# Performance work log

Measured on AMD Instinct MI355X. Metric: run time of the kernel, lower is better.

The kernel has to match this reference:

```python
import jax, jax.numpy as jnp
import numpy as np

NUM_EXPERTS = 8
TOP_K = 2


def setup_inputs() -> dict:
    key = jax.random.key(0)
    ks = jax.random.split(key, 5)
    B, L, E, H, N = 2, 2048, 1024, 2048, NUM_EXPERTS
    return {
        "x": jax.random.normal(ks[0], (B, L, E), dtype=jnp.float32),
        "gate_kernel": jax.random.normal(ks[1], (E, N), dtype=jnp.float32) / np.sqrt(E),
        "w0_kernel": jax.random.normal(ks[2], (N, E, H), dtype=jnp.float32) / np.sqrt(E),
        "w1_kernel": jax.random.normal(ks[3], (N, E, H), dtype=jnp.float32) / np.sqrt(E),
        "wo_kernel": jax.random.normal(ks[4], (N, H, E), dtype=jnp.float32) / np.sqrt(H),
    }


def reference(x, gate_kernel, w0_kernel, w1_kernel, wo_kernel):
    B, L, E = x.shape
    # Router: [B, L, N]
    gate_logits = jnp.einsum("ble,en->bln", x, gate_kernel)
    top_k_weights, top_k_indices = jax.lax.top_k(gate_logits, TOP_K)
    # softmax over the selected top-k logits (in fp32, as in original)
    softmax_probs = jax.nn.softmax(top_k_weights.astype(jnp.float32), axis=-1)
    # scatter probs back into dense [B, L, N] routing weights
    weights = jnp.zeros_like(gate_logits)
    b_idx = jnp.arange(B)[:, None, None]
    l_idx = jnp.arange(L)[:, None]
    weights = weights.at[b_idx, l_idx, top_k_indices].set(softmax_probs)
    # Dense all-experts FFN (as in the original module)
    layer_w0 = jnp.einsum("ble,neh->blnh", x, w0_kernel)  # [B,L,N,H]
    layer_w1 = jnp.einsum("ble,neh->blnh", x, w1_kernel)
    layer_mult = jax.nn.silu(layer_w0) * layer_w1
    intermediate = jnp.einsum("blnh,nhe->blne", layer_mult, wo_kernel)
    output = jnp.einsum("blne,bln->ble", intermediate, weights)
    return output
```

## Files before the change

kernel.cpp:

```cpp
#include <hip/hip_runtime.h>
#include <stdint.h>


#define T_TOKENS 4096
#define E_DIM 1024
#define H_DIM 2048
#define BM 128
#define BN 64
#define BK 32
#define MAX_TILES 72

typedef __attribute__((ext_vector_type(8))) short bf16x8;
typedef __attribute__((ext_vector_type(8))) unsigned short u16x8;
typedef __attribute__((ext_vector_type(4))) float f32x4;

__device__ __forceinline__ unsigned short f2bf(float f) {
  unsigned u = __float_as_uint(f);
  u += 0x7fff + ((u >> 16) & 1);
  return (unsigned short)(u >> 16);
}

__device__ __forceinline__ void gll16(const void* g, void* l) {
  __builtin_amdgcn_global_load_lds(
      (__attribute__((address_space(1))) void*)(uintptr_t)g,
      (__attribute__((address_space(3))) void*)l, 16, 0, 0);
}

__global__ __launch_bounds__(256) void router_kernel(
    const float* __restrict__ x, const float* __restrict__ gate,
    int* __restrict__ cnt, int2* __restrict__ tok_e,
    int2* __restrict__ tok_pos, float2* __restrict__ tok_w,
    unsigned short* __restrict__ xb) {
  int lane = threadIdx.x & 63;
  int wv = threadIdx.x >> 6;
  int t = blockIdx.x * 4 + wv;
  const float* xr = x + (size_t)t * E_DIM;
  unsigned short* xbr = xb + (size_t)t * E_DIM;
  float acc[8];
#pragma unroll
  for (int n = 0; n < 8; n++) acc[n] = 0.f;
#pragma unroll
  for (int i = 0; i < 16; i++) {
    int k = i * 64 + lane;
    float xv = xr[k];
    xbr[k] = f2bf(xv);
    const float4* gp = (const float4*)(gate + (size_t)k * 8);
    float4 g0 = gp[0], g1 = gp[1];
    acc[0] += xv * g0.x; acc[1] += xv * g0.y;
    acc[2] += xv * g0.z; acc[3] += xv * g0.w;
    acc[4] += xv * g1.x; acc[5] += xv * g1.y;
    acc[6] += xv * g1.z; acc[7] += xv * g1.w;
  }
#pragma unroll
  for (int s = 32; s >= 1; s >>= 1) {
#pragma unroll
    for (int n = 0; n < 8; n++) acc[n] += __shfl_xor(acc[n], s, 64);
  }
  if (lane == 0) {
    int i0 = 0; float v0 = acc[0];
#pragma unroll
    for (int n = 1; n < 8; n++) if (acc[n] > v0) { v0 = acc[n]; i0 = n; }
    int i1 = -1; float v1 = -3.4e38f;
#pragma unroll
    for (int n = 0; n < 8; n++) if (n != i0 && acc[n] > v1) { v1 = acc[n]; i1 = n; }
    float e1 = __expf(v1 - v0);
    float inv = 1.f / (1.f + e1);
    int p0 = atomicAdd(&cnt[i0], 1);
    int p1 = atomicAdd(&cnt[i1], 1);
    tok_e[t] = make_int2(i0, i1);
    tok_pos[t] = make_int2(p0, p1);
    tok_w[t] = make_float2(inv, e1 * inv);
  }
}

__global__ __launch_bounds__(256) void scatter_kernel(
    const int* __restrict__ cnt, const int2* __restrict__ tok_e,
    const int2* __restrict__ tok_pos, int* __restrict__ tlist,
    int2* __restrict__ tok_slot) {
  int t = blockIdx.x * 256 + threadIdx.x;
  if (t >= T_TOKENS) return;
  int offs[8]; int a = 0;
#pragma unroll
  for (int e = 0; e < 8; e++) { offs[e] = a; a += cnt[e]; }
  int2 te = tok_e[t]; int2 tp = tok_pos[t];
  int s0 = offs[te.x] + tp.x, s1 = offs[te.y] + tp.y;
  tlist[s0] = t; tlist[s1] = t;
  tok_slot[t] = make_int2(s0, s1);
}

__global__ __launch_bounds__(256) void transpose_convert_kernel(
    const float* __restrict__ src, unsigned short* __restrict__ dst, int R, int C) {
  __shared__ float tile[64][65];
  size_t bofs = (size_t)blockIdx.z * R * C;
  const float* s = src + bofs;
  unsigned short* d = dst + bofs;
  int r0 = blockIdx.y * 64, c0 = blockIdx.x * 64;
  int tr = threadIdx.x >> 2;
  int tc = (threadIdx.x & 3) * 16;
  const float* sp = s + (size_t)(r0 + tr) * C + c0 + tc;
#pragma unroll
  for (int j = 0; j < 4; j++) {
    float4 v = ((const float4*)sp)[j];
    tile[tr][tc + j * 4 + 0] = v.x; tile[tr][tc + j * 4 + 1] = v.y;
    tile[tr][tc + j * 4 + 2] = v.z; tile[tr][tc + j * 4 + 3] = v.w;
  }
  __syncthreads();
  int co = tr;
  int rc = tc;
  u16x8 o0, o1;
#pragma unroll
  for (int j = 0; j < 8; j++) o0[j] = f2bf(tile[rc + j][co]);
#pragma unroll
  for (int j = 0; j < 8; j++) o1[j] = f2bf(tile[rc + 8 + j][co]);
  unsigned short* dp = d + (size_t)(c0 + co) * R + r0 + rc;
  *(u16x8*)dp = o0;
  *(u16x8*)(dp + 8) = o1;
}

__device__ __forceinline__ bool map_tile(const int* cnt, int tile, int& eSel,
                                         int& slot0, int& rows) {
  eSel = -1;
  int acc = 0, off = 0;
  for (int e = 0; e < 8; e++) {
    int ce = cnt[e];
    int te = (ce + BM - 1) / BM;
    if (eSel < 0 && tile < acc + te) {
      eSel = e;
      int tin = tile - acc;
      slot0 = off + tin * BM;
      rows = min(BM, ce - tin * BM);
    }
    acc += te; off += ce;
  }
  return eSel >= 0;
}

__global__ __launch_bounds__(256, 3) void gemm1_kernel(
    const unsigned short* __restrict__ xb,
    const unsigned short* __restrict__ w0t,
    const unsigned short* __restrict__ w1t,
    const int* __restrict__ cnt, const int* __restrict__ tlist,
    unsigned short* __restrict__ Mbuf) {
  __shared__ alignas(16) unsigned short As[BM * BK];
  __shared__ alignas(16) unsigned short B0s[BN * BK];
  __shared__ alignas(16) unsigned short B1s[BN * BK];

  int eSel, slot0, rows;
  if (!map_tile(cnt, blockIdx.y, eSel, slot0, rows)) return;
  int h0 = blockIdx.x * BN;

  int tid = threadIdx.x, lane = tid & 63, wv = tid >> 6;
  int sr = lane >> 2;
  int colE = (lane & 3) * 8;
  int ar0 = wv * 32 + sr, ar1 = ar0 + 16;
  int ra0 = min(ar0, rows - 1), ra1 = min(ar1, rows - 1);
  const unsigned short* aS0 = xb + (size_t)tlist[slot0 + ra0] * E_DIM + colE;
  const unsigned short* aS1 = xb + (size_t)tlist[slot0 + ra1] * E_DIM + colE;
  int br = wv * 16 + sr;
  const unsigned short* b0S = w0t + ((size_t)eSel * H_DIM + h0 + br) * E_DIM + colE;
  const unsigned short* b1S = w1t + ((size_t)eSel * H_DIM + h0 + br) * E_DIM + colE;

  f32x4 acc0[4][2], acc1[4][2];
  f32x4 fz = {0.f, 0.f, 0.f, 0.f};
#pragma unroll
  for (int m = 0; m < 4; m++)
#pragma unroll
    for (int n = 0; n < 2; n++) { acc0[m][n] = fz; acc1[m][n] = fz; }

  unsigned short* As_w = &As[wv * 1024];
  unsigned short* B0s_w = &B0s[wv * 512];
  unsigned short* B1s_w = &B1s[wv * 512];
  int rbase = (wv >> 1) * 64, cbase = (wv & 1) * 32;
  int fr = lane & 15, fk = (lane >> 4) * 8;

  for (int k0 = 0; k0 < E_DIM; k0 += BK) {
    gll16(aS0 + k0, As_w);
    gll16(aS1 + k0, As_w + 512);
    gll16(b0S + k0, B0s_w);
    gll16(b1S + k0, B1s_w);
    __syncthreads();
    bf16x8 a[4], b0[2], b1[2];
#pragma unroll
    for (int m = 0; m < 4; m++)
      a[m] = *(const bf16x8*)&As[(rbase + m * 16 + fr) * BK + fk];
#pragma unroll
    for (int n = 0; n < 2; n++) {
      b0[n] = *(const bf16x8*)&B0s[(cbase + n * 16 + fr) * BK + fk];
      b1[n] = *(const bf16x8*)&B1s[(cbase + n * 16 + fr) * BK + fk];
    }
#pragma unroll
    for (int m = 0; m < 4; m++)
#pragma unroll
      for (int n = 0; n < 2; n++) {
        acc0[m][n] = __builtin_amdgcn_mfma_f32_16x16x32_bf16(a[m], b0[n], acc0[m][n], 0, 0, 0);
        acc1[m][n] = __builtin_amdgcn_mfma_f32_16x16x32_bf16(a[m], b1[n], acc1[m][n], 0, 0, 0);
      }
    __syncthreads();
  }
  int rj = (lane >> 4) * 4;
#pragma unroll
  for (int m = 0; m < 4; m++) {
#pragma unroll
    for (int j = 0; j < 4; j++) {
      int r = rbase + m * 16 + rj + j;
      if (r < rows) {
        size_t rowp = (size_t)(slot0 + r) * H_DIM + h0 + cbase + fr;
#pragma unroll
        for (int n = 0; n < 2; n++) {
          float v0 = acc0[m][n][j], v1 = acc1[m][n][j];
          float mv = v0 / (1.f + __expf(-v0)) * v1;
          Mbuf[rowp + n * 16] = f2bf(mv);
        }
      }
    }
  }
}

__global__ __launch_bounds__(256, 4) void gemm2_kernel(
    const unsigned short* __restrict__ Mbuf,
    const unsigned short* __restrict__ wot,
    const int* __restrict__ cnt,
    float* __restrict__ Obuf) {
  __shared__ alignas(16) unsigned short As[BM * BK];
  __shared__ alignas(16) unsigned short Bs[BN * BK];

  int eSel, slot0, rows;
  if (!map_tile(cnt, blockIdx.y, eSel, slot0, rows)) return;
  int eo0 = blockIdx.x * BN;

  int tid = threadIdx.x, lane = tid & 63, wv = tid >> 6;
  int sr = lane >> 2;
  int colE = (lane & 3) * 8;
  int ar0 = wv * 32 + sr, ar1 = ar0 + 16;
  int ra0 = min(ar0, rows - 1), ra1 = min(ar1, rows - 1);
  const unsigned short* aS0 = Mbuf + (size_t)(slot0 + ra0) * H_DIM + colE;
  const unsigned short* aS1 = Mbuf + (size_t)(slot0 + ra1) * H_DIM + colE;
  int br = wv * 16 + sr;
  const unsigned short* bS = wot + ((size_t)eSel * E_DIM + eo0 + br) * H_DIM + colE;

  f32x4 acc[4][2];
  f32x4 fz = {0.f, 0.f, 0.f, 0.f};
#pragma unroll
  for (int m = 0; m < 4; m++)
#pragma unroll
    for (int n = 0; n < 2; n++) acc[m][n] = fz;

  unsigned short* As_w = &As[wv * 1024];
  unsigned short* Bs_w = &Bs[wv * 512];
  int rbase = (wv >> 1) * 64, cbase = (wv & 1) * 32;
  int fr = lane & 15, fk = (lane >> 4) * 8;

  for (int k0 = 0; k0 < H_DIM; k0 += BK) {
    gll16(aS0 + k0, As_w);
    gll16(aS1 + k0, As_w + 512);
    gll16(bS + k0, Bs_w);
    __syncthreads();
    bf16x8 a[4], b[2];
#pragma unroll
    for (int m = 0; m < 4; m++)
      a[m] = *(const bf16x8*)&As[(rbase + m * 16 + fr) * BK + fk];
#pragma unroll
    for (int n = 0; n < 2; n++)
      b[n] = *(const bf16x8*)&Bs[(cbase + n * 16 + fr) * BK + fk];
#pragma unroll
    for (int m = 0; m < 4; m++)
#pragma unroll
      for (int n = 0; n < 2; n++)
        acc[m][n] = __builtin_amdgcn_mfma_f32_16x16x32_bf16(a[m], b[n], acc[m][n], 0, 0, 0);
    __syncthreads();
  }
  int rj = (lane >> 4) * 4;
#pragma unroll
  for (int m = 0; m < 4; m++) {
#pragma unroll
    for (int j = 0; j < 4; j++) {
      int r = rbase + m * 16 + rj + j;
      if (r < rows) {
        size_t rowp = (size_t)(slot0 + r) * E_DIM + eo0 + cbase + fr;
#pragma unroll
        for (int n = 0; n < 2; n++) Obuf[rowp + n * 16] = acc[m][n][j];
      }
    }
  }
}

__global__ __launch_bounds__(256) void combine_kernel(
    const float* __restrict__ Obuf, const int2* __restrict__ tok_slot,
    const float2* __restrict__ tok_w, float* __restrict__ out) {
  int t = blockIdx.x;
  int c = threadIdx.x * 4;
  int2 s = tok_slot[t];
  float2 wgt = tok_w[t];
  float4 a = *(const float4*)(Obuf + (size_t)s.x * E_DIM + c);
  float4 b = *(const float4*)(Obuf + (size_t)s.y * E_DIM + c);
  float4 o;
  o.x = wgt.x * a.x + wgt.y * b.x;
  o.y = wgt.x * a.y + wgt.y * b.y;
  o.z = wgt.x * a.z + wgt.y * b.z;
  o.w = wgt.x * a.w + wgt.y * b.w;
  *(float4*)(out + (size_t)t * E_DIM + c) = o;
}

extern "C" void kernel_launch(void* const* d_in, const int* in_sizes, int n_in,
                              void* d_out, int out_size, void* d_ws, size_t ws_size,
                              hipStream_t stream) {
  (void)in_sizes; (void)n_in; (void)out_size; (void)ws_size;
  const float* x = (const float*)d_in[0];
  const float* gate = (const float*)d_in[1];
  const float* w0 = (const float*)d_in[2];
  const float* w1 = (const float*)d_in[3];
  const float* wo = (const float*)d_in[4];
  float* out = (float*)d_out;
  char* ws = (char*)d_ws;

  int* cnt = (int*)(ws + 0);
  int2* tok_e = (int2*)(ws + 256);
  int2* tok_pos = (int2*)(ws + 256 + 32768);
  float2* tok_w = (float2*)(ws + 256 + 2 * 32768);
  int2* tok_slot = (int2*)(ws + 256 + 3 * 32768);
  int* tlist = (int*)(ws + 256 + 4 * 32768);
  size_t o = 256 + 5 * 32768;
  unsigned short* xb = (unsigned short*)(ws + o);  o += (size_t)T_TOKENS * E_DIM * 2;
  unsigned short* w0t = (unsigned short*)(ws + o); o += (size_t)8 * H_DIM * E_DIM * 2;
  unsigned short* w1t = (unsigned short*)(ws + o); o += (size_t)8 * H_DIM * E_DIM * 2;
  unsigned short* wot = (unsigned short*)(ws + o); o += (size_t)8 * E_DIM * H_DIM * 2;
  unsigned short* Mbuf = (unsigned short*)(ws + o); o += (size_t)8192 * H_DIM * 2;
  float* Obuf = (float*)w0t;

  hipMemsetAsync(cnt, 0, 32, stream);
  hipLaunchKernelGGL(router_kernel, dim3(1024), dim3(256), 0, stream,
                     x, gate, cnt, tok_e, tok_pos, tok_w, xb);
  hipLaunchKernelGGL(scatter_kernel, dim3(16), dim3(256), 0, stream,
                     cnt, tok_e, tok_pos, tlist, tok_slot);
  hipLaunchKernelGGL(transpose_convert_kernel, dim3(32, 16, 8), dim3(256), 0, stream,
                     w0, w0t, E_DIM, H_DIM);
  hipLaunchKernelGGL(transpose_convert_kernel, dim3(32, 16, 8), dim3(256), 0, stream,
                     w1, w1t, E_DIM, H_DIM);
  hipLaunchKernelGGL(transpose_convert_kernel, dim3(16, 32, 8), dim3(256), 0, stream,
                     wo, wot, H_DIM, E_DIM);
  hipLaunchKernelGGL(gemm1_kernel, dim3(32, MAX_TILES), dim3(256), 0, stream,
                     xb, w0t, w1t, cnt, tlist, Mbuf);
  hipLaunchKernelGGL(gemm2_kernel, dim3(16, MAX_TILES), dim3(256), 0, stream,
                     Mbuf, wot, cnt, Obuf);
  hipLaunchKernelGGL(combine_kernel, dim3(4096), dim3(256), 0, stream,
                     Obuf, tok_slot, tok_w, out);
}
```

Baseline: 501.2 us.

## Fuse combine into gemm2 via atomics, widen BK with swizzled LDS, vectorize router

```diff
diff --git a/kernel.cpp b/kernel.cpp
--- a/kernel.cpp
+++ b/kernel.cpp
@@ -6,8 +6,7 @@
 #define E_DIM 1024
 #define H_DIM 2048
 #define BM 128
-#define BN 64
-#define BK 32
+#define BK 64
 #define MAX_TILES 72
 
 typedef __attribute__((ext_vector_type(8))) short bf16x8;
@@ -25,6 +24,7 @@
       (__attribute__((address_space(1))) void*)(uintptr_t)g,
       (__attribute__((address_space(3))) void*)l, 16, 0, 0);
 }
+
 
 __global__ __launch_bounds__(256) void router_kernel(
     const float* __restrict__ x, const float* __restrict__ gate,
@@ -40,16 +40,22 @@
 #pragma unroll
   for (int n = 0; n < 8; n++) acc[n] = 0.f;
 #pragma unroll
-  for (int i = 0; i < 16; i++) {
-    int k = i * 64 + lane;
-    float xv = xr[k];
-    xbr[k] = f2bf(xv);
-    const float4* gp = (const float4*)(gate + (size_t)k * 8);
-    float4 g0 = gp[0], g1 = gp[1];
-    acc[0] += xv * g0.x; acc[1] += xv * g0.y;
-    acc[2] += xv * g0.z; acc[3] += xv * g0.w;
-    acc[4] += xv * g1.x; acc[5] += xv * g1.y;
-    acc[6] += xv * g1.z; acc[7] += xv * g1.w;
+  for (int i = 0; i < 4; i++) {
+    int k4 = i * 256 + lane * 4;
+    float4 xv = *(const float4*)(xr + k4);
+    ushort4 ov;
+    ov.x = f2bf(xv.x); ov.y = f2bf(xv.y); ov.z = f2bf(xv.z); ov.w = f2bf(xv.w);
+    *(ushort4*)(xbr + k4) = ov;
+    float xa[4] = {xv.x, xv.y, xv.z, xv.w};
+#pragma unroll
+    for (int c = 0; c < 4; c++) {
+      const float4* gp = (const float4*)(gate + (size_t)(k4 + c) * 8);
+      float4 g0 = gp[0], g1 = gp[1];
+      acc[0] += xa[c] * g0.x; acc[1] += xa[c] * g0.y;
+      acc[2] += xa[c] * g0.z; acc[3] += xa[c] * g0.w;
+      acc[4] += xa[c] * g1.x; acc[5] += xa[c] * g1.y;
+      acc[6] += xa[c] * g1.z; acc[7] += xa[c] * g1.w;
+    }
   }
 #pragma unroll
   for (int s = 32; s >= 1; s >>= 1) {
@@ -75,17 +81,18 @@
 
 __global__ __launch_bounds__(256) void scatter_kernel(
     const int* __restrict__ cnt, const int2* __restrict__ tok_e,
-    const int2* __restrict__ tok_pos, int* __restrict__ tlist,
-    int2* __restrict__ tok_slot) {
+    const int2* __restrict__ tok_pos, const float2* __restrict__ tok_w,
+    int* __restrict__ tlist, float* __restrict__ wlist) {
   int t = blockIdx.x * 256 + threadIdx.x;
   if (t >= T_TOKENS) return;
   int offs[8]; int a = 0;
 #pragma unroll
   for (int e = 0; e < 8; e++) { offs[e] = a; a += cnt[e]; }
   int2 te = tok_e[t]; int2 tp = tok_pos[t];
+  float2 w = tok_w[t];
   int s0 = offs[te.x] + tp.x, s1 = offs[te.y] + tp.y;
   tlist[s0] = t; tlist[s1] = t;
-  tok_slot[t] = make_int2(s0, s1);
+  wlist[s0] = w.x; wlist[s1] = w.y;
 }
 
 __global__ __launch_bounds__(256) void transpose_convert_kernel(
@@ -142,23 +149,32 @@
     const int* __restrict__ cnt, const int* __restrict__ tlist,
     unsigned short* __restrict__ Mbuf) {
   __shared__ alignas(16) unsigned short As[BM * BK];
-  __shared__ alignas(16) unsigned short B0s[BN * BK];
-  __shared__ alignas(16) unsigned short B1s[BN * BK];
+  __shared__ alignas(16) unsigned short B0s[64 * BK];
+  __shared__ alignas(16) unsigned short B1s[64 * BK];
 
   int eSel, slot0, rows;
   if (!map_tile(cnt, blockIdx.y, eSel, slot0, rows)) return;
-  int h0 = blockIdx.x * BN;
+  int h0 = blockIdx.x * 64;
 
   int tid = threadIdx.x, lane = tid & 63, wv = tid >> 6;
-  int sr = lane >> 2;
-  int colE = (lane & 3) * 8;
-  int ar0 = wv * 32 + sr, ar1 = ar0 + 16;
-  int ra0 = min(ar0, rows - 1), ra1 = min(ar1, rows - 1);
-  const unsigned short* aS0 = xb + (size_t)tlist[slot0 + ra0] * E_DIM + colE;
-  const unsigned short* aS1 = xb + (size_t)tlist[slot0 + ra1] * E_DIM + colE;
-  int br = wv * 16 + sr;
-  const unsigned short* b0S = w0t + ((size_t)eSel * H_DIM + h0 + br) * E_DIM + colE;
-  const unsigned short* b1S = w1t + ((size_t)eSel * H_DIM + h0 + br) * E_DIM + colE;
+  int lr = lane >> 3;
+  int swz = ((lane & 7) ^ lr) * 8;
+
+  const unsigned short* aP[4];
+#pragma unroll
+  for (int j = 0; j < 4; j++) {
+    int r = wv * 32 + j * 8 + lr;
+    int rc = min(r, rows - 1);
+    aP[j] = xb + (size_t)tlist[slot0 + rc] * E_DIM + swz;
+  }
+  const unsigned short* b0P[2];
+  const unsigned short* b1P[2];
+#pragma unroll
+  for (int j = 0; j < 2; j++) {
+    int hr = h0 + wv * 16 + j * 8 + lr;
+    b0P[j] = w0t + ((size_t)eSel * H_DIM + hr) * E_DIM + swz;
+    b1P[j] = w1t + ((size_t)eSel * H_DIM + hr) * E_DIM + swz;
+  }
 
   f32x4 acc0[4][2], acc1[4][2];
   f32x4 fz = {0.f, 0.f, 0.f, 0.f};
@@ -167,37 +183,44 @@
 #pragma unroll
     for (int n = 0; n < 2; n++) { acc0[m][n] = fz; acc1[m][n] = fz; }
 
-  unsigned short* As_w = &As[wv * 1024];
-  unsigned short* B0s_w = &B0s[wv * 512];
-  unsigned short* B1s_w = &B1s[wv * 512];
+  unsigned short* AsW = &As[wv * 2048];
+  unsigned short* B0W = &B0s[wv * 1024];
+  unsigned short* B1W = &B1s[wv * 1024];
   int rbase = (wv >> 1) * 64, cbase = (wv & 1) * 32;
-  int fr = lane & 15, fk = (lane >> 4) * 8;
+  int fr = lane & 15, q = lane >> 4, fx = fr & 7;
 
   for (int k0 = 0; k0 < E_DIM; k0 += BK) {
-    gll16(aS0 + k0, As_w);
-    gll16(aS1 + k0, As_w + 512);
-    gll16(b0S + k0, B0s_w);
-    gll16(b1S + k0, B1s_w);
+#pragma unroll
+    for (int j = 0; j < 4; j++) gll16(aP[j] + k0, AsW + j * 512);
+#pragma unroll
+    for (int j = 0; j < 2; j++) {
+      gll16(b0P[j] + k0, B0W + j * 512);
+      gll16(b1P[j] + k0, B1W + j * 512);
+    }
     __syncthreads();
-    bf16x8 a[4], b0[2], b1[2];
-#pragma unroll
-    for (int m = 0; m < 4; m++)
-      a[m] = *(const bf16x8*)&As[(rbase + m * 16 + fr) * BK + fk];
-#pragma unroll
-    for (int n = 0; n < 2; n++) {
-      b0[n] = *(const bf16x8*)&B0s[(cbase + n * 16 + fr) * BK + fk];
-      b1[n] = *(const bf16x8*)&B1s[(cbase + n * 16 + fr) * BK + fk];
-    }
-#pragma unroll
-    for (int m = 0; m < 4; m++)
+#pragma unroll
+    for (int kk = 0; kk < 2; kk++) {
+      int so = ((kk * 4 + q) ^ fx) * 8;
+      bf16x8 a[4], b0[2], b1[2];
+#pragma unroll
+      for (int m = 0; m < 4; m++)
+        a[m] = *(const bf16x8*)&As[(rbase + m * 16 + fr) * BK + so];
 #pragma unroll
       for (int n = 0; n < 2; n++) {
-        acc0[m][n] = __builtin_amdgcn_mfma_f32_16x16x32_bf16(a[m], b0[n], acc0[m][n], 0, 0, 0);
-        acc1[m][n] = __builtin_amdgcn_mfma_f32_16x16x32_bf16(a[m], b1[n], acc1[m][n], 0, 0, 0);
+        b0[n] = *(const bf16x8*)&B0s[(cbase + n * 16 + fr) * BK + so];
+        b1[n] = *(const bf16x8*)&B1s[(cbase + n * 16 + fr) * BK + so];
       }
+#pragma unroll
+      for (int m = 0; m < 4; m++)
+#pragma unroll
+        for (int n = 0; n < 2; n++) {
+          acc0[m][n] = __builtin_amdgcn_mfma_f32_16x16x32_bf16(a[m], b0[n], acc0[m][n], 0, 0, 0);
+          acc1[m][n] = __builtin_amdgcn_mfma_f32_16x16x32_bf16(a[m], b1[n], acc1[m][n], 0, 0, 0);
+        }
+    }
     __syncthreads();
   }
-  int rj = (lane >> 4) * 4;
+  int rj = q * 4;
 #pragma unroll
   for (int m = 0; m < 4; m++) {
 #pragma unroll
@@ -216,89 +239,87 @@
   }
 }
 
-__global__ __launch_bounds__(256, 4) void gemm2_kernel(
+__global__ __launch_bounds__(256, 3) void gemm2_kernel(
     const unsigned short* __restrict__ Mbuf,
     const unsigned short* __restrict__ wot,
-    const int* __restrict__ cnt,
-    float* __restrict__ Obuf) {
+    const int* __restrict__ cnt, const int* __restrict__ tlist,
+    const float* __restrict__ wlist,
+    float* __restrict__ out) {
   __shared__ alignas(16) unsigned short As[BM * BK];
-  __shared__ alignas(16) unsigned short Bs[BN * BK];
+  __shared__ alignas(16) unsigned short Bs[BM * BK];
 
   int eSel, slot0, rows;
   if (!map_tile(cnt, blockIdx.y, eSel, slot0, rows)) return;
-  int eo0 = blockIdx.x * BN;
+  int eo0 = blockIdx.x * 128;
 
   int tid = threadIdx.x, lane = tid & 63, wv = tid >> 6;
-  int sr = lane >> 2;
-  int colE = (lane & 3) * 8;
-  int ar0 = wv * 32 + sr, ar1 = ar0 + 16;
-  int ra0 = min(ar0, rows - 1), ra1 = min(ar1, rows - 1);
-  const unsigned short* aS0 = Mbuf + (size_t)(slot0 + ra0) * H_DIM + colE;
-  const unsigned short* aS1 = Mbuf + (size_t)(slot0 + ra1) * H_DIM + colE;
-  int br = wv * 16 + sr;
-  const unsigned short* bS = wot + ((size_t)eSel * E_DIM + eo0 + br) * H_DIM + colE;
-
-  f32x4 acc[4][2];
+  int lr = lane >> 3;
+  int swz = ((lane & 7) ^ lr) * 8;
+
+  const unsigned short* aP[4];
+  const unsigned short* bP[4];
+#pragma unroll
+  for (int j = 0; j < 4; j++) {
+    int r = wv * 32 + j * 8 + lr;
+    int rc = min(r, rows - 1);
+    aP[j] = Mbuf + (size_t)(slot0 + rc) * H_DIM + swz;
+    bP[j] = wot + ((size_t)eSel * E_DIM + eo0 + r) * H_DIM + swz;
+  }
+
+  f32x4 acc[4][4];
   f32x4 fz = {0.f, 0.f, 0.f, 0.f};
 #pragma unroll
   for (int m = 0; m < 4; m++)
 #pragma unroll
-    for (int n = 0; n < 2; n++) acc[m][n] = fz;
-
-  unsigned short* As_w = &As[wv * 1024];
-  unsigned short* Bs_w = &Bs[wv * 512];
-  int rbase = (wv >> 1) * 64, cbase = (wv & 1) * 32;
-  int fr = lane & 15, fk = (lane >> 4) * 8;
+    for (int n = 0; n < 4; n++) acc[m][n] = fz;
+
+  unsigned short* AsW = &As[wv * 2048];
+  unsigned short* BsW = &Bs[wv * 2048];
+  int rbase = (wv >> 1) * 64, cbase = (wv & 1) * 64;
+  int fr = lane & 15, q = lane >> 4, fx = fr & 7;
 
   for (int k0 = 0; k0 < H_DIM; k0 += BK) {
-    gll16(aS0 + k0, As_w);
-    gll16(aS1 + k0, As_w + 512);
-    gll16(bS + k0, Bs_w);
+#pragma unroll
+    for (int j = 0; j < 4; j++) {
+      gll16(aP[j] + k0, AsW + j * 512);
+      gll16(bP[j] + k0, BsW + j * 512);
+    }
     __syncthreads();
-    bf16x8 a[4], b[2];
-#pragma unroll
-    for (int m = 0; m < 4; m++)
-      a[m] = *(const bf16x8*)&As[(rbase + m * 16 + fr) * BK + fk];
-#pragma unroll
-    for (int n = 0; n < 2; n++)
-      b[n] = *(const bf16x8*)&Bs[(cbase + n * 16 + fr) * BK + fk];
-#pragma unroll
-    for (int m = 0; m < 4; m++)
-#pragma unroll
-      for (int n = 0; n < 2; n++)
-        acc[m][n] = __builtin_amdgcn_mfma_f32_16x16x32_bf16(a[m], b[n], acc[m][n], 0, 0, 0);
+#pragma unroll
+    for (int kk = 0; kk < 2; kk++) {
+      int so = ((kk * 4 + q) ^ fx) * 8;
+      bf16x8 a[4], b[4];
+#pragma unroll
+      for (int m = 0; m < 4; m++)
+        a[m] = *(const bf16x8*)&As[(rbase + m * 16 + fr) * BK + so];
+#pragma unroll
+      for (int n = 0; n < 4; n++)
+        b[n] = *(const bf16x8*)&Bs[(cbase + n * 16 + fr) * BK + so];
+#pragma unroll
+      for (int m = 0; m < 4; m++)
+#pragma unroll
+        for (int n = 0; n < 4; n++)
+          acc[m][n] = __builtin_amdgcn_mfma_f32_16x16x32_bf16(a[m], b[n], acc[m][n], 0, 0, 0);
+    }
     __syncthreads();
   }
-  int rj = (lane >> 4) * 4;
+  int rj = q * 4;
 #pragma unroll
   for (int m = 0; m < 4; m++) {
 #pragma unroll
     for (int j = 0; j < 4; j++) {
       int r = rbase + m * 16 + rj + j;
       if (r < rows) {
-        size_t rowp = (size_t)(slot0 + r) * E_DIM + eo0 + cbase + fr;
-#pragma unroll
-        for (int n = 0; n < 2; n++) Obuf[rowp + n * 16] = acc[m][n][j];
+        int s = slot0 + r;
+        int tok = tlist[s];
+        float w = wlist[s];
+        float* orow = out + (size_t)tok * E_DIM + eo0 + cbase + fr;
+#pragma unroll
+        for (int n = 0; n < 4; n++)
+          atomicAdd(orow + n * 16, w * acc[m][n][j]);
       }
     }
   }
-}
-
-__global__ __launch_bounds__(256) void combine_kernel(
-    const float* __restrict__ Obuf, const int2* __restrict__ tok_slot,
-    const float2* __restrict__ tok_w, float* __restrict__ out) {
-  int t = blockIdx.x;
-  int c = threadIdx.x * 4;
-  int2 s = tok_slot[t];
-  float2 wgt = tok_w[t];
-  float4 a = *(const float4*)(Obuf + (size_t)s.x * E_DIM + c);
-  float4 b = *(const float4*)(Obuf + (size_t)s.y * E_DIM + c);
-  float4 o;
-  o.x = wgt.x * a.x + wgt.y * b.x;
-  o.y = wgt.x * a.y + wgt.y * b.y;
-  o.z = wgt.x * a.z + wgt.y * b.z;
-  o.w = wgt.x * a.w + wgt.y * b.w;
-  *(float4*)(out + (size_t)t * E_DIM + c) = o;
 }
 
 extern "C" void kernel_launch(void* const* d_in, const int* in_sizes, int n_in,
@@ -317,21 +338,21 @@
   int2* tok_e = (int2*)(ws + 256);
   int2* tok_pos = (int2*)(ws + 256 + 32768);
   float2* tok_w = (float2*)(ws + 256 + 2 * 32768);
-  int2* tok_slot = (int2*)(ws + 256 + 3 * 32768);
-  int* tlist = (int*)(ws + 256 + 4 * 32768);
+  int* tlist = (int*)(ws + 256 + 3 * 32768);
+  float* wlist = (float*)(ws + 256 + 4 * 32768);
   size_t o = 256 + 5 * 32768;
   unsigned short* xb = (unsigned short*)(ws + o);  o += (size_t)T_TOKENS * E_DIM * 2;
   unsigned short* w0t = (unsigned short*)(ws + o); o += (size_t)8 * H_DIM * E_DIM * 2;
   unsigned short* w1t = (unsigned short*)(ws + o); o += (size_t)8 * H_DIM * E_DIM * 2;
   unsigned short* wot = (unsigned short*)(ws + o); o += (size_t)8 * E_DIM * H_DIM * 2;
   unsigned short* Mbuf = (unsigned short*)(ws + o); o += (size_t)8192 * H_DIM * 2;
-  float* Obuf = (float*)w0t;
 
   hipMemsetAsync(cnt, 0, 32, stream);
+  hipMemsetAsync(out, 0, (size_t)T_TOKENS * E_DIM * 4, stream);
   hipLaunchKernelGGL(router_kernel, dim3(1024), dim3(256), 0, stream,
                      x, gate, cnt, tok_e, tok_pos, tok_w, xb);
   hipLaunchKernelGGL(scatter_kernel, dim3(16), dim3(256), 0, stream,
-                     cnt, tok_e, tok_pos, tlist, tok_slot);
+                     cnt, tok_e, tok_pos, tok_w, tlist, wlist);
   hipLaunchKernelGGL(transpose_convert_kernel, dim3(32, 16, 8), dim3(256), 0, stream,
                      w0, w0t, E_DIM, H_DIM);
   hipLaunchKernelGGL(transpose_convert_kernel, dim3(32, 16, 8), dim3(256), 0, stream,
@@ -340,8 +361,6 @@
                      wo, wot, H_DIM, E_DIM);
   hipLaunchKernelGGL(gemm1_kernel, dim3(32, MAX_TILES), dim3(256), 0, stream,
                      xb, w0t, w1t, cnt, tlist, Mbuf);
-  hipLaunchKernelGGL(gemm2_kernel, dim3(16, MAX_TILES), dim3(256), 0, stream,
-                     Mbuf, wot, cnt, Obuf);
-  hipLaunchKernelGGL(combine_kernel, dim3(4096), dim3(256), 0, stream,
-                     Obuf, tok_slot, tok_w, out);
-}
+  hipLaunchKernelGGL(gemm2_kernel, dim3(8, MAX_TILES), dim3(256), 0, stream,
+                     Mbuf, wot, cnt, tlist, wlist, out);
+}
```

Result: faster. 490.0 us (-2.2%).
